# Optimization experiments

Hardware: AMD Instinct MI355X
Metric: run time of the kernel (lower is better)

Reference implementation:

```python
import jax, jax.numpy as jnp
import numpy as np

DISCOUNT_FACTOR = 0.99
EPS = 1e-8


def setup_inputs() -> dict:
    key = jax.random.key(0)
    k1, k2, k3 = jax.random.split(key, 3)
    B, S = 8192, 1024
    # raw params initialized exactly like the torch module: atanh(target)
    raw_gamma = jnp.arctanh(jnp.array([DISCOUNT_FACTOR], dtype=jnp.float32))
    # create_init_lambda_sequence(0.5, S): linear ramp with mean == AVERAGE_LAMBDA
    lam_init = jnp.linspace(0.1, 0.9, S).astype(jnp.float32)
    raw_lambd = jnp.arctanh(lam_init)
    values = jax.random.normal(k1, (B, S + 1, 1), dtype=jnp.float32)
    rewards = jax.random.normal(k2, (B, S, 1), dtype=jnp.float32)
    dones = jax.random.randint(k3, (B, S, 1), 0, 2).astype(jnp.int32)
    return {
        "raw_gamma": raw_gamma,
        "raw_lambd": raw_lambd,
        "values": values,
        "rewards": rewards,
        "dones": dones,
        "input_seq_len": 1024,
    }


def reference(raw_gamma, raw_lambd, values, rewards, dones, input_seq_len):
    # gamma / lambd properties: tanh then clamp_min(1e-8)
    gamma = jnp.maximum(jnp.tanh(raw_gamma), EPS)[0]            # scalar
    lambd = jnp.maximum(jnp.tanh(raw_lambd), EPS)               # [max_seq_len]
    lam_seq = lambd[-input_seq_len:]                            # [S]

    # ---- update_sum_reward_weights (runs under no_grad in torch) ----
    # backward recurrence: v[t] = gamma * (1 - lam[t] + lam[t] * v[t+1]),  v[S] = 1
    def w_step(v_next, lam_t):
        v_t = gamma * (1.0 - lam_t + lam_t * v_next)
        return v_t, jnp.maximum(1.0 - v_t, EPS)

    _, w = jax.lax.scan(
        w_step,
        jnp.asarray(1.0, values.dtype),
        jax.lax.stop_gradient(lam_seq),
        reverse=True,
    )  # w: [S]
    srw = w / jnp.maximum(w.mean(), EPS)
    sum_reward_weights = jax.lax.stop_gradient(srw)[None, :, None]  # [1, S, 1]

    # ---- calculate_lambda_returns ----
    # ret[t] = r[t] + gamma*(1-done[t]) * ((1-lam[t])*V[t+1] + lam[t]*ret[t+1])
    d = dones.astype(values.dtype)
    v_next = values[:, 1:, :]                                   # [B, S, 1]
    xs = (
        jnp.swapaxes(rewards, 0, 1),   # [S, B, 1]
        jnp.swapaxes(d, 0, 1),         # [S, B, 1]
        jnp.swapaxes(v_next, 0, 1),    # [S, B, 1]
        lam_seq,                       # [S]
    )

    def r_step(ret_next, x):
        r, dn, vn, lam = x
        ret = r + gamma * (1.0 - dn) * ((1.0 - lam) * vn + lam * ret_next)
        return ret, ret

    _, rets = jax.lax.scan(r_step, values[:, -1, :], xs, reverse=True)  # [S, B, 1]
    lambda_returns = jnp.swapaxes(rets, 0, 1)                           # [B, S, 1]
    return lambda_returns, sum_reward_weights
```

## Files before the change

kernel.cpp:

```cpp
#include <hip/hip_runtime.h>
#include <math.h>

#define EPSF 1e-8f

typedef float fvec4 __attribute__((ext_vector_type(4), aligned(4)));
typedef float nvec4 __attribute__((ext_vector_type(4)));

__device__ __forceinline__ void suffix_scan64(float& A, float& B, int lane) {
#pragma unroll
    for (int d = 1; d < 64; d <<= 1) {
        float Ao = __shfl_down(A, d);
        float Bo = __shfl_down(B, d);
        if (lane + d < 64) {
            A = fmaf(B, Ao, A);
            B = B * Bo;
        }
    }
}

__global__ __launch_bounds__(256, 4)
void td_kernel(const float* __restrict__ raw_gamma,
               const float* __restrict__ raw_lambd, int lam_off,
               const float* __restrict__ values,
               const float* __restrict__ rewards,
               const int* __restrict__ dones,
               float* __restrict__ out,
               int B, int S, int rowBlocks)
{
    __shared__ float s_gl[1024];
    __shared__ float s_gol[1024];
    const float gamma = fmaxf(tanhf(raw_gamma[0]), EPSF);
    for (int t = threadIdx.x; t < S; t += 256) {
        float lam = fmaxf(tanhf(raw_lambd[lam_off + t]), EPSF);
        float g1 = gamma * lam;
        s_gl[t] = g1;
        s_gol[t] = gamma - g1;
    }
    __syncthreads();

    const int lane = threadIdx.x & 63;

    if ((int)blockIdx.x == rowBlocks) {
        if (threadIdx.x >= 64) return;
        const int base = lane << 4;
        float a[16], b[16];
#pragma unroll
        for (int j = 0; j < 16; ++j) { a[j] = s_gol[base + j]; b[j] = s_gl[base + j]; }
        float A = a[15], Bc = b[15];
#pragma unroll
        for (int j = 14; j >= 0; --j) { A = fmaf(b[j], A, a[j]); Bc *= b[j]; }
        suffix_scan64(A, Bc, lane);
        float EA = __shfl_down(A, 1);
        float EB = __shfl_down(Bc, 1);
        if (lane == 63) { EA = 0.0f; EB = 1.0f; }
        float v = EA + EB;
        float w[16], sum = 0.0f;
#pragma unroll
        for (int j = 15; j >= 0; --j) {
            v = fmaf(b[j], v, a[j]);
            w[j] = fmaxf(1.0f - v, EPSF);
            sum += w[j];
        }
#pragma unroll
        for (int d = 32; d; d >>= 1) sum += __shfl_xor(sum, d);
        float inv = 1.0f / fmaxf(sum / (float)S, EPSF);
        float* srw = out + (size_t)B * S;
#pragma unroll
        for (int j = 0; j < 16; ++j) srw[base + j] = w[j] * inv;
        return;
    }

    const int b = blockIdx.x * 4 + (threadIdx.x >> 6);
    if (b >= B) return;
    const int C = S >> 2;
    const int t0 = lane << 2;

    const float* rrow = rewards + (size_t)b * S;
    const int*   drow = dones   + (size_t)b * S;
    const float* vrow = values  + (size_t)b * (S + 1);
    float*       orow = out     + (size_t)b * S;

    float4 r4[4]; int4 d4[4]; fvec4 v4[4];
#pragma unroll
    for (int c = 0; c < 4; ++c) {
        int t = c * C + t0;
        r4[c] = *(const float4*)(rrow + t);
        d4[c] = *(const int4*)(drow + t);
        v4[c] = *(const fvec4*)(vrow + t + 1);
    }
    float vS = vrow[S];

    float a[16], bb[16];
#pragma unroll
    for (int c = 0; c < 4; ++c) {
        const float4 G1 = *(const float4*)&s_gl[c * C + t0];
        const float4 G0 = *(const float4*)&s_gol[c * C + t0];
        float vn[4] = {v4[c].x, v4[c].y, v4[c].z, v4[c].w};
        float rr[4] = {r4[c].x, r4[c].y, r4[c].z, r4[c].w};
        int   di[4] = {d4[c].x, d4[c].y, d4[c].z, d4[c].w};
        float g1v[4] = {G1.x, G1.y, G1.z, G1.w};
        float g0v[4] = {G0.x, G0.y, G0.z, G0.w};
#pragma unroll
        for (int j = 0; j < 4; ++j) {
            float nd = 1.0f - (float)di[j];
            bb[c * 4 + j] = g1v[j] * nd;
            a[c * 4 + j]  = fmaf(g0v[j] * vn[j], nd, rr[j]);
        }
    }

    float A[4], Bc[4];
#pragma unroll
    for (int c = 0; c < 4; ++c) {
        A[c] = a[c * 4 + 3]; Bc[c] = bb[c * 4 + 3];
#pragma unroll
        for (int j = 2; j >= 0; --j) {
            A[c] = fmaf(bb[c * 4 + j], A[c], a[c * 4 + j]);
            Bc[c] *= bb[c * 4 + j];
        }
    }

#pragma unroll
    for (int d = 1; d < 64; d <<= 1) {
        float Ao[4], Bo[4];
#pragma unroll
        for (int c = 0; c < 4; ++c) {
            Ao[c] = __shfl_down(A[c], d);
            Bo[c] = __shfl_down(Bc[c], d);
        }
        if (lane + d < 64) {
#pragma unroll
            for (int c = 0; c < 4; ++c) {
                A[c] = fmaf(Bc[c], Ao[c], A[c]);
                Bc[c] *= Bo[c];
            }
        }
    }

    float EA[4], EB[4], A0[4], B0[4];
#pragma unroll
    for (int c = 0; c < 4; ++c) {
        EA[c] = __shfl_down(A[c], 1);
        EB[c] = __shfl_down(Bc[c], 1);
        A0[c] = __shfl(A[c], 0);
        B0[c] = __shfl(Bc[c], 0);
    }
    if (lane == 63) {
#pragma unroll
        for (int c = 0; c < 4; ++c) { EA[c] = 0.0f; EB[c] = 1.0f; }
    }

    float x4 = vS;
    float x3 = fmaf(B0[3], x4, A0[3]);
    float x2 = fmaf(B0[2], x3, A0[2]);
    float x1 = fmaf(B0[1], x2, A0[1]);
    float xin[4] = {x1, x2, x3, x4};

#pragma unroll
    for (int c = 0; c < 4; ++c) {
        float x  = fmaf(EB[c], xin[c], EA[c]);
        float o3 = fmaf(bb[c * 4 + 3], x,  a[c * 4 + 3]);
        float o2 = fmaf(bb[c * 4 + 2], o3, a[c * 4 + 2]);
        float o1 = fmaf(bb[c * 4 + 1], o2, a[c * 4 + 1]);
        float o0 = fmaf(bb[c * 4 + 0], o1, a[c * 4 + 0]);
        nvec4 ov = {o0, o1, o2, o3};
        __builtin_nontemporal_store(ov, (nvec4*)(orow + c * C + t0));
    }
}

extern "C" void kernel_launch(void* const* d_in, const int* in_sizes, int n_in,
                              void* d_out, int out_size, void* d_ws, size_t ws_size,
                              hipStream_t stream) {
    const float* raw_gamma = (const float*)d_in[0];
    const float* raw_lambd = (const float*)d_in[1];
    const float* values    = (const float*)d_in[2];
    const float* rewards   = (const float*)d_in[3];
    const int*   dones     = (const int*)d_in[4];
    float* out = (float*)d_out;

    int n_v = in_sizes[2];
    int n_r = in_sizes[3];
    int B = n_v - n_r;
    int S = n_r / B;
    int lam_off = in_sizes[1] - S;

    int rowBlocks = (B + 3) / 4;
    td_kernel<<<rowBlocks + 1, 256, 0, stream>>>(
        raw_gamma, raw_lambd, lam_off, values, rewards, dones,
        out, B, S, rowBlocks);
}
```

Before: 146.8 us.

## Process four rows per wave with register double-buffered prefetch

Each wavefront now handles four consecutive batch rows instead of one and loads the next row's rewards, dones and values into registers while it scans the current row. This spreads the per-block tanh/LDS setup over more rows and overlaps global loads with the shuffle scan. The second LDS array is dropped and gamma-g1 is recomputed in registers. The launch bound is loosened to 2 blocks per CU to make room for the extra registers. In exchange the grid shrinks fourfold, occupancy may fall, and latency hiding now rests on the explicit prefetch.

```diff
diff --git a/kernel.cpp b/kernel.cpp
--- a/kernel.cpp
+++ b/kernel.cpp
@@ -18,7 +18,7 @@
     }
 }
 
-__global__ __launch_bounds__(256, 4)
+__global__ __launch_bounds__(256, 2)
 void td_kernel(const float* __restrict__ raw_gamma,
                const float* __restrict__ raw_lambd, int lam_off,
                const float* __restrict__ values,
@@ -28,14 +28,9 @@
                int B, int S, int rowBlocks)
 {
     __shared__ float s_gl[1024];
-    __shared__ float s_gol[1024];
     const float gamma = fmaxf(tanhf(raw_gamma[0]), EPSF);
-    for (int t = threadIdx.x; t < S; t += 256) {
-        float lam = fmaxf(tanhf(raw_lambd[lam_off + t]), EPSF);
-        float g1 = gamma * lam;
-        s_gl[t] = g1;
-        s_gol[t] = gamma - g1;
-    }
+    for (int t = threadIdx.x; t < S; t += 256)
+        s_gl[t] = gamma * fmaxf(tanhf(raw_lambd[lam_off + t]), EPSF);
     __syncthreads();
 
     const int lane = threadIdx.x & 63;
@@ -45,7 +40,7 @@
         const int base = lane << 4;
         float a[16], b[16];
 #pragma unroll
-        for (int j = 0; j < 16; ++j) { a[j] = s_gol[base + j]; b[j] = s_gl[base + j]; }
+        for (int j = 0; j < 16; ++j) { b[j] = s_gl[base + j]; a[j] = gamma - b[j]; }
         float A = a[15], Bc = b[15];
 #pragma unroll
         for (int j = 14; j >= 0; --j) { A = fmaf(b[j], A, a[j]); Bc *= b[j]; }
@@ -70,100 +65,127 @@
         return;
     }
 
-    const int b = blockIdx.x * 4 + (threadIdx.x >> 6);
-    if (b >= B) return;
     const int C = S >> 2;
     const int t0 = lane << 2;
-
-    const float* rrow = rewards + (size_t)b * S;
-    const int*   drow = dones   + (size_t)b * S;
-    const float* vrow = values  + (size_t)b * (S + 1);
-    float*       orow = out     + (size_t)b * S;
-
-    float4 r4[4]; int4 d4[4]; fvec4 v4[4];
-#pragma unroll
-    for (int c = 0; c < 4; ++c) {
-        int t = c * C + t0;
-        r4[c] = *(const float4*)(rrow + t);
-        d4[c] = *(const int4*)(drow + t);
-        v4[c] = *(const fvec4*)(vrow + t + 1);
-    }
-    float vS = vrow[S];
-
-    float a[16], bb[16];
-#pragma unroll
-    for (int c = 0; c < 4; ++c) {
-        const float4 G1 = *(const float4*)&s_gl[c * C + t0];
-        const float4 G0 = *(const float4*)&s_gol[c * C + t0];
-        float vn[4] = {v4[c].x, v4[c].y, v4[c].z, v4[c].w};
-        float rr[4] = {r4[c].x, r4[c].y, r4[c].z, r4[c].w};
-        int   di[4] = {d4[c].x, d4[c].y, d4[c].z, d4[c].w};
-        float g1v[4] = {G1.x, G1.y, G1.z, G1.w};
-        float g0v[4] = {G0.x, G0.y, G0.z, G0.w};
-#pragma unroll
-        for (int j = 0; j < 4; ++j) {
-            float nd = 1.0f - (float)di[j];
-            bb[c * 4 + j] = g1v[j] * nd;
-            a[c * 4 + j]  = fmaf(g0v[j] * vn[j], nd, rr[j]);
-        }
-    }
-
-    float A[4], Bc[4];
-#pragma unroll
-    for (int c = 0; c < 4; ++c) {
-        A[c] = a[c * 4 + 3]; Bc[c] = bb[c * 4 + 3];
-#pragma unroll
-        for (int j = 2; j >= 0; --j) {
-            A[c] = fmaf(bb[c * 4 + j], A[c], a[c * 4 + j]);
-            Bc[c] *= bb[c * 4 + j];
-        }
-    }
-
-#pragma unroll
-    for (int d = 1; d < 64; d <<= 1) {
-        float Ao[4], Bo[4];
-#pragma unroll
-        for (int c = 0; c < 4; ++c) {
-            Ao[c] = __shfl_down(A[c], d);
-            Bo[c] = __shfl_down(Bc[c], d);
-        }
-        if (lane + d < 64) {
+    const int b0 = (blockIdx.x * 4 + (threadIdx.x >> 6)) * 4;
+    if (b0 >= B) return;
+
+    float4 G1[4];
+#pragma unroll
+    for (int c = 0; c < 4; ++c) G1[c] = *(const float4*)&s_gl[c * C + t0];
+
+    float4 cr[4]; int4 cd[4]; fvec4 cv[4]; float cvS;
+    {
+        const float* rrow = rewards + (size_t)b0 * S;
+        const int*   drow = dones   + (size_t)b0 * S;
+        const float* vrow = values  + (size_t)b0 * (S + 1);
+#pragma unroll
+        for (int c = 0; c < 4; ++c) {
+            int t = c * C + t0;
+            cr[c] = *(const float4*)(rrow + t);
+            cd[c] = *(const int4*)(drow + t);
+            cv[c] = *(const fvec4*)(vrow + t + 1);
+        }
+        cvS = vrow[S];
+    }
+
+#pragma unroll 1
+    for (int r = 0; r < 4; ++r) {
+        const int b = b0 + r;
+        float4 nr[4]; int4 nd[4]; fvec4 nv[4]; float nvS = 0.0f;
+        if (r < 3 && b + 1 < B) {
+            const float* rrow = rewards + (size_t)(b + 1) * S;
+            const int*   drow = dones   + (size_t)(b + 1) * S;
+            const float* vrow = values  + (size_t)(b + 1) * (S + 1);
 #pragma unroll
             for (int c = 0; c < 4; ++c) {
-                A[c] = fmaf(Bc[c], Ao[c], A[c]);
-                Bc[c] *= Bo[c];
-            }
-        }
-    }
-
-    float EA[4], EB[4], A0[4], B0[4];
-#pragma unroll
-    for (int c = 0; c < 4; ++c) {
-        EA[c] = __shfl_down(A[c], 1);
-        EB[c] = __shfl_down(Bc[c], 1);
-        A0[c] = __shfl(A[c], 0);
-        B0[c] = __shfl(Bc[c], 0);
-    }
-    if (lane == 63) {
-#pragma unroll
-        for (int c = 0; c < 4; ++c) { EA[c] = 0.0f; EB[c] = 1.0f; }
-    }
-
-    float x4 = vS;
-    float x3 = fmaf(B0[3], x4, A0[3]);
-    float x2 = fmaf(B0[2], x3, A0[2]);
-    float x1 = fmaf(B0[1], x2, A0[1]);
-    float xin[4] = {x1, x2, x3, x4};
-
-#pragma unroll
-    for (int c = 0; c < 4; ++c) {
-        float x  = fmaf(EB[c], xin[c], EA[c]);
-        float o3 = fmaf(bb[c * 4 + 3], x,  a[c * 4 + 3]);
-        float o2 = fmaf(bb[c * 4 + 2], o3, a[c * 4 + 2]);
-        float o1 = fmaf(bb[c * 4 + 1], o2, a[c * 4 + 1]);
-        float o0 = fmaf(bb[c * 4 + 0], o1, a[c * 4 + 0]);
-        nvec4 ov = {o0, o1, o2, o3};
-        __builtin_nontemporal_store(ov, (nvec4*)(orow + c * C + t0));
+                int t = c * C + t0;
+                nr[c] = *(const float4*)(rrow + t);
+                nd[c] = *(const int4*)(drow + t);
+                nv[c] = *(const fvec4*)(vrow + t + 1);
+            }
+            nvS = vrow[S];
+        }
+
+        float a[16], bb[16];
+#pragma unroll
+        for (int c = 0; c < 4; ++c) {
+            float vn[4] = {cv[c].x, cv[c].y, cv[c].z, cv[c].w};
+            float rr[4] = {cr[c].x, cr[c].y, cr[c].z, cr[c].w};
+            int   di[4] = {cd[c].x, cd[c].y, cd[c].z, cd[c].w};
+            float g1v[4] = {G1[c].x, G1[c].y, G1[c].z, G1[c].w};
+#pragma unroll
+            for (int j = 0; j < 4; ++j) {
+                float nd_ = 1.0f - (float)di[j];
+                bb[c * 4 + j] = g1v[j] * nd_;
+                a[c * 4 + j]  = fmaf((gamma - g1v[j]) * vn[j], nd_, rr[j]);
+            }
+        }
+
+        float A[4], Bc[4];
+#pragma unroll
+        for (int c = 0; c < 4; ++c) {
+            A[c] = a[c * 4 + 3]; Bc[c] = bb[c * 4 + 3];
+#pragma unroll
+            for (int j = 2; j >= 0; --j) {
+                A[c] = fmaf(bb[c * 4 + j], A[c], a[c * 4 + j]);
+                Bc[c] *= bb[c * 4 + j];
+            }
+        }
+
+#pragma unroll
+        for (int d = 1; d < 64; d <<= 1) {
+            float Ao[4], Bo[4];
+#pragma unroll
+            for (int c = 0; c < 4; ++c) {
+                Ao[c] = __shfl_down(A[c], d);
+                Bo[c] = __shfl_down(Bc[c], d);
+            }
+            if (lane + d < 64) {
+#pragma unroll
+                for (int c = 0; c < 4; ++c) {
+                    A[c] = fmaf(Bc[c], Ao[c], A[c]);
+                    Bc[c] *= Bo[c];
+                }
+            }
+        }
+
+        float EA[4], EB[4], A0[4], B0[4];
+#pragma unroll
+        for (int c = 0; c < 4; ++c) {
+            EA[c] = __shfl_down(A[c], 1);
+            EB[c] = __shfl_down(Bc[c], 1);
+            A0[c] = __shfl(A[c], 0);
+            B0[c] = __shfl(Bc[c], 0);
+        }
+        if (lane == 63) {
+#pragma unroll
+            for (int c = 0; c < 4; ++c) { EA[c] = 0.0f; EB[c] = 1.0f; }
+        }
+
+        float x4 = cvS;
+        float x3 = fmaf(B0[3], x4, A0[3]);
+        float x2 = fmaf(B0[2], x3, A0[2]);
+        float x1 = fmaf(B0[1], x2, A0[1]);
+        float xin[4] = {x1, x2, x3, x4};
+
+        float* orow = out + (size_t)b * S;
+#pragma unroll
+        for (int c = 0; c < 4; ++c) {
+            float x  = fmaf(EB[c], xin[c], EA[c]);
+            float o3 = fmaf(bb[c * 4 + 3], x,  a[c * 4 + 3]);
+            float o2 = fmaf(bb[c * 4 + 2], o3, a[c * 4 + 2]);
+            float o1 = fmaf(bb[c * 4 + 1], o2, a[c * 4 + 1]);
+            float o0 = fmaf(bb[c * 4 + 0], o1, a[c * 4 + 0]);
+            nvec4 ov = {o0, o1, o2, o3};
+            __builtin_nontemporal_store(ov, (nvec4*)(orow + c * C + t0));
+        }
+
+        if (r < 3) {
+#pragma unroll
+            for (int c = 0; c < 4; ++c) { cr[c] = nr[c]; cd[c] = nd[c]; cv[c] = nv[c]; }
+            cvS = nvS;
+        }
     }
 }
 
@@ -183,7 +205,7 @@
     int S = n_r / B;
     int lam_off = in_sizes[1] - S;
 
-    int rowBlocks = (B + 3) / 4;
+    int rowBlocks = (B + 15) / 16;
     td_kernel<<<rowBlocks + 1, 256, 0, stream>>>(
         raw_gamma, raw_lambd, lam_off, values, rewards, dones,
         out, B, S, rowBlocks);
```

Result: no change. 144.8 us (-1.4%).
